# Kernel optimization log

Measured on AMD Instinct MI355X. Metric: run time of the kernel, lower is better.

The kernel has to match this reference:

```python
import jax, jax.numpy as jnp
import numpy as np

N = 50000      # nodes
E = 800000     # edges (before self-loops)
IN = 128       # input_dim
H = 4          # heads in conv1
C = 128        # per-head channels
G = 128        # num graphs in batch
OUT = 8        # output_dim
EPS = 1e-5


def layer_norm(x, g, b):
    mu = jnp.mean(x, axis=-1, keepdims=True)
    var = jnp.var(x, axis=-1, keepdims=True)
    return (x - mu) * jax.lax.rsqrt(var + EPS) * g + b


def gat_conv(x, src, dst, W, att_src, att_dst, bias, heads, ch):
    n = x.shape[0]
    h = (x @ W).reshape(n, heads, ch)                      # [N,H,C]
    a_src = jnp.einsum('nhc,hc->nh', h, att_src)           # [N,H]
    a_dst = jnp.einsum('nhc,hc->nh', h, att_dst)
    e = jax.nn.leaky_relu(a_src[src] + a_dst[dst], 0.2)    # [E,H]
    e_max = jax.ops.segment_max(e, dst, num_segments=n)
    e_max = jnp.where(jnp.isfinite(e_max), e_max, 0.0)
    ex = jnp.exp(e - e_max[dst])
    denom = jax.ops.segment_sum(ex, dst, num_segments=n)
    alpha = ex / (denom[dst] + 1e-16)                      # segment softmax over dst
    msg = h[src] * alpha[:, :, None]                       # [E,H,C]
    out = jax.ops.segment_sum(msg, dst, num_segments=n)    # [N,H,C]
    return out.reshape(n, heads * ch) + bias


def _forward(x, edge_index, batch, params):
    (W1, as1, ad1, b1, g1, be1, W2, as2, ad2, b2, g2, be2,
     rW1, rb1, rg, rbe, rW2, rb2) = params
    # add self-loops (PyG GATConv default)
    loop = jnp.arange(N)
    src = jnp.concatenate([edge_index[0], loop])
    dst = jnp.concatenate([edge_index[1], loop])
    h1 = jax.nn.relu(layer_norm(gat_conv(x, src, dst, W1, as1, ad1, b1, H, C), g1, be1))
    h2 = jax.nn.relu(layer_norm(gat_conv(h1, src, dst, W2, as2, ad2, b2, 1, C), g2, be2))
    # global mean pool
    sums = jax.ops.segment_sum(h2, batch, num_segments=G)
    cnt = jax.ops.segment_sum(jnp.ones((N, 1), h2.dtype), batch, num_segments=G)
    pooled = sums / jnp.maximum(cnt, 1.0)
    r = jax.nn.relu(layer_norm(pooled @ rW1 + rb1, rg, rbe))
    return r @ rW2 + rb2                                   # [G, OUT]


def setup_inputs() -> dict:
    key = jax.random.key(0)
    ks = jax.random.split(key, 24)
    s = 0.05
    return {
        'x': jax.random.normal(ks[0], (N, IN), jnp.float32),
        'edge_index': jax.random.randint(ks[1], (2, E), 0, N),
        'edge_weight': jax.random.uniform(ks[2], (E,), jnp.float32),
        'batch': jnp.sort(jax.random.randint(ks[3], (N,), 0, G)),
        'W1': jax.random.normal(ks[4], (IN, H * C), jnp.float32) * s,
        'att_src1': jax.random.normal(ks[5], (H, C), jnp.float32) * s,
        'att_dst1': jax.random.normal(ks[6], (H, C), jnp.float32) * s,
        'b1': jnp.zeros((H * C,), jnp.float32),
        'g1': jnp.ones((H * C,), jnp.float32),
        'be1': jnp.zeros((H * C,), jnp.float32),
        'W2': jax.random.normal(ks[7], (H * C, C), jnp.float32) * s,
        'att_src2': jax.random.normal(ks[8], (1, C), jnp.float32) * s,
        'att_dst2': jax.random.normal(ks[9], (1, C), jnp.float32) * s,
        'b2': jnp.zeros((C,), jnp.float32),
        'g2': jnp.ones((C,), jnp.float32),
        'be2': jnp.zeros((C,), jnp.float32),
        'rW1': jax.random.normal(ks[10], (C, 32), jnp.float32) * s,
        'rb1': jnp.zeros((32,), jnp.float32),
        'rg': jnp.ones((32,), jnp.float32),
        'rbe': jnp.zeros((32,), jnp.float32),
        'rW2': jax.random.normal(ks[11], (32, OUT), jnp.float32) * s,
        'rb2': jnp.zeros((OUT,), jnp.float32),
    }


def reference(x, edge_index, edge_weight, batch, W1, att_src1, att_dst1, b1, g1, be1,
              W2, att_src2, att_dst2, b2, g2, be2, rW1, rb1, rg, rbe, rW2, rb2):
    # edge_weight is accepted but unused, matching the original forward
    params = (W1, att_src1, att_dst1, b1, g1, be1, W2, att_src2, att_dst2, b2, g2, be2,
              rW1, rb1, rg, rbe, rW2, rb2)
    return _forward(x, edge_index, batch, params)
```

## Files before the change

kernel.cpp:

```cpp
#include <hip/hip_runtime.h>
#include <math.h>

#define HEADS 4
#define CH 128
#define HC 512
#define GRAPHS 128
#define OUT_DIM 8

typedef unsigned short u16;
typedef unsigned int u32;
typedef short short8 __attribute__((ext_vector_type(8)));
typedef float f32x4 __attribute__((ext_vector_type(4)));

__device__ inline u16 f2b(float f) {
  u32 u = __float_as_uint(f);
  u32 r = u + 0x7FFFu + ((u >> 16) & 1u);
  return (u16)(r >> 16);
}
__device__ inline float blo(u32 d) { return __uint_as_float(d << 16); }
__device__ inline float bhi(u32 d) { return __uint_as_float(d & 0xffff0000u); }
__device__ inline float lrelu(float v) { return v > 0.f ? v : 0.2f * v; }
__device__ inline int rdl(int v, int l) { return __builtin_amdgcn_readlane(v, l); }
__device__ inline float rdlf(float v, int l) {
  return __int_as_float(__builtin_amdgcn_readlane(__float_as_int(v), l));
}

__global__ void k_count(const int* __restrict__ ei, int* __restrict__ counts, int E, int N) {
  int i = blockIdx.x * blockDim.x + threadIdx.x;
  int total = E + N;
  if (i >= total) return;
  int dst = (i < E) ? ei[E + i] : (i - E);
  atomicAdd(&counts[dst], 1);
}

__global__ __launch_bounds__(256) void k_scanA(const int* __restrict__ counts,
                                               int* __restrict__ bsum, int N) {
  __shared__ int sh[256];
  int b = blockIdx.x, t = threadIdx.x, i = b * 256 + t;
  sh[t] = (i < N) ? counts[i] : 0;
  __syncthreads();
  for (int off = 128; off; off >>= 1) {
    if (t < off) sh[t] += sh[t + off];
    __syncthreads();
  }
  if (t == 0) bsum[b] = sh[0];
}

__global__ __launch_bounds__(1024) void k_scanB(const int* __restrict__ bsum,
                                                int* __restrict__ boff, int nb) {
  __shared__ int sh[1024];
  int t = threadIdx.x;
  sh[t] = (t < nb) ? bsum[t] : 0;
  __syncthreads();
  for (int off = 1; off < 1024; off <<= 1) {
    int v = sh[t];
    int u = (t >= off) ? sh[t - off] : 0;
    __syncthreads();
    sh[t] = v + u;
    __syncthreads();
  }
  if (t < nb) boff[t] = (t == 0) ? 0 : sh[t - 1];
}

__global__ __launch_bounds__(256) void k_scanC(const int* __restrict__ counts,
                                               const int* __restrict__ boff,
                                               int* __restrict__ indptr,
                                               int* __restrict__ cursor, int N) {
  __shared__ int sh[256];
  int b = blockIdx.x, t = threadIdx.x, i = b * 256 + t;
  int v = (i < N) ? counts[i] : 0;
  sh[t] = v;
  __syncthreads();
  for (int off = 1; off < 256; off <<= 1) {
    int a = sh[t];
    int u = (t >= off) ? sh[t - off] : 0;
    __syncthreads();
    sh[t] = a + u;
    __syncthreads();
  }
  if (i < N) {
    int excl = boff[b] + sh[t] - v;
    indptr[i] = excl;
    cursor[i] = excl;
    if (i == N - 1) indptr[N] = excl + v;
  }
}

__global__ void k_scatter(const int* __restrict__ ei, int* __restrict__ cursor,
                          int* __restrict__ srcs, int E, int N) {
  int i = blockIdx.x * blockDim.x + threadIdx.x;
  int total = E + N;
  if (i >= total) return;
  int src, dst;
  if (i < E) { src = ei[i]; dst = ei[E + i]; } else { src = i - E; dst = i - E; }
  int pos = atomicAdd(&cursor[dst], 1);
  srcs[pos] = src;
}

__global__ void k_wt(const float* __restrict__ W, u16* __restrict__ Wt, int K, int Nc) {
  int i = blockIdx.x * blockDim.x + threadIdx.x;
  if (i >= K * Nc) return;
  int n = i / K, k = i - n * K;
  Wt[i] = f2b(W[(size_t)k * Nc + n]);
}

__global__ __launch_bounds__(256) void k_ws(const float* __restrict__ W1,
                                            const float* __restrict__ as1,
                                            const float* __restrict__ ad1,
                                            float* __restrict__ ws) {
  int t = threadIdx.x;
  #pragma unroll
  for (int r = 0; r < 4; r++) {
    int idx = r * 256 + t;
    int k = idx >> 3, o = idx & 7, h = o & 3;
    const float* av = ((o < 4) ? as1 : ad1) + h * CH;
    const float* wrow = W1 + (size_t)k * HC + h * CH;
    float s = 0.f;
    for (int c = 0; c < CH; c++) s += wrow[c] * av[c];
    ws[idx] = s;
  }
}

__global__ void k_prep(const float* __restrict__ x, const float* __restrict__ ws,
                       u32* __restrict__ xb, float4* __restrict__ sa1,
                       float4* __restrict__ da1, int N) {
  int n = blockIdx.x * (blockDim.x >> 6) + (threadIdx.x >> 6);
  int lane = threadIdx.x & 63;
  if (n >= N) return;
  float2 v = ((const float2*)(x + (size_t)n * 128))[lane];
  xb[(size_t)n * 64 + lane] = (u32)f2b(v.x) | ((u32)f2b(v.y) << 16);
  const float* w0 = ws + (2 * lane) * 8;
  const float* w1 = ws + (2 * lane + 1) * 8;
  float p[8];
  #pragma unroll
  for (int o = 0; o < 8; o++) p[o] = v.x * w0[o] + v.y * w1[o];
  #pragma unroll
  for (int off = 32; off; off >>= 1)
    #pragma unroll
    for (int o = 0; o < 8; o++) p[o] += __shfl_xor(p[o], off);
  if (lane == 0) {
    sa1[n] = make_float4(p[0], p[1], p[2], p[3]);
    da1[n] = make_float4(p[4], p[5], p[6], p[7]);
  }
}

__global__ __launch_bounds__(256) void k_aggx(
    const u32* __restrict__ xb, const int* __restrict__ indptr,
    const int* __restrict__ srcs, const float4* __restrict__ as1,
    const float4* __restrict__ ad1, u32* __restrict__ aggx, int N) {
  int t = threadIdx.x;
  int lane = t & 63, wid = t >> 6;
  int n0 = blockIdx.x * 8 + wid * 2;
  if (n0 >= N) return;
  int n1 = n0 + 1;
  bool has1 = n1 < N;
  int beg0 = indptr[n0], end0 = indptr[n0 + 1];
  int beg1 = end0, end1 = has1 ? indptr[n1 + 1] : end0;
  int deg0 = end0 - beg0, deg1 = end1 - beg1;
  float4 ad0 = ad1[n0];
  float4 adv1 = has1 ? ad1[n1] : make_float4(0.f, 0.f, 0.f, 0.f);

  if (deg0 <= 64 && deg1 <= 64) {
    int s0 = 0, s1 = 0;
    float w0[4] = {}, w1[4] = {};
    if (lane < deg0) {
      s0 = srcs[beg0 + lane];
      float4 a = as1[s0];
      w0[0] = __expf(lrelu(a.x + ad0.x)); w0[1] = __expf(lrelu(a.y + ad0.y));
      w0[2] = __expf(lrelu(a.z + ad0.z)); w0[3] = __expf(lrelu(a.w + ad0.w));
    }
    if (lane < deg1) {
      s1 = srcs[beg1 + lane];
      float4 a = as1[s1];
      w1[0] = __expf(lrelu(a.x + adv1.x)); w1[1] = __expf(lrelu(a.y + adv1.y));
      w1[2] = __expf(lrelu(a.z + adv1.z)); w1[3] = __expf(lrelu(a.w + adv1.w));
    }
    float e0[4] = {}, e1[4] = {};
    float c0[4][2] = {}, c1[4][2] = {};
    int dmax = deg0 > deg1 ? deg0 : deg1;
    int dpad = (dmax + 3) & ~3;
    for (int j = 0; j < dpad; j += 4) {
      u32 d[4], e[4];
      #pragma unroll
      for (int u = 0; u < 4; u++) d[u] = xb[(size_t)rdl(s0, j + u) * 64 + lane];
      #pragma unroll
      for (int u = 0; u < 4; u++) e[u] = xb[(size_t)rdl(s1, j + u) * 64 + lane];
      #pragma unroll
      for (int h = 0; h < 4; h++) {
        #pragma unroll
        for (int u = 0; u < 4; u++) {
          float a = rdlf(w0[h], j + u);
          e0[h] += a; c0[h][0] += a * blo(d[u]); c0[h][1] += a * bhi(d[u]);
          float b = rdlf(w1[h], j + u);
          e1[h] += b; c1[h][0] += b * blo(e[u]); c1[h][1] += b * bhi(e[u]);
        }
      }
    }
    {
      u32* orow = aggx + (size_t)n0 * 256;
      #pragma unroll
      for (int h = 0; h < 4; h++) {
        float iv = 1.f / (e0[h] + 1e-16f);
        orow[h * 64 + lane] = (u32)f2b(c0[h][0] * iv) | ((u32)f2b(c0[h][1] * iv) << 16);
      }
    }
    if (has1) {
      u32* orow = aggx + (size_t)n1 * 256;
      #pragma unroll
      for (int h = 0; h < 4; h++) {
        float iv = 1.f / (e1[h] + 1e-16f);
        orow[h * 64 + lane] = (u32)f2b(c1[h][0] * iv) | ((u32)f2b(c1[h][1] * iv) << 16);
      }
    }
    return;
  }
  for (int pass = 0; pass < 2; pass++) {
    if (pass == 1 && !has1) break;
    int n = pass ? n1 : n0;
    int beg = pass ? beg1 : beg0;
    int end = pass ? end1 : end0;
    float4 ad = pass ? adv1 : ad0;
    float e0[4] = {};
    float c0[4][2] = {};
    for (int base = beg; base < end; base += 64) {
      int cnt = min(64, end - base);
      int sreg = 0;
      float w0[4] = {};
      if (lane < cnt) {
        sreg = srcs[base + lane];
        float4 a = as1[sreg];
        w0[0] = __expf(lrelu(a.x + ad.x)); w0[1] = __expf(lrelu(a.y + ad.y));
        w0[2] = __expf(lrelu(a.z + ad.z)); w0[3] = __expf(lrelu(a.w + ad.w));
      }
      int cpad = (cnt + 1) & ~1;
      for (int j = 0; j < cpad; j += 2) {
        u32 dA = xb[(size_t)rdl(sreg, j) * 64 + lane];
        u32 dB = xb[(size_t)rdl(sreg, j + 1) * 64 + lane];
        float xA0 = blo(dA), xA1 = bhi(dA), xB0 = blo(dB), xB1 = bhi(dB);
        #pragma unroll
        for (int h = 0; h < 4; h++) {
          float a = rdlf(w0[h], j), b = rdlf(w0[h], j + 1);
          e0[h] += a + b;
          c0[h][0] += a * xA0 + b * xB0;
          c0[h][1] += a * xA1 + b * xB1;
        }
      }
    }
    u32* orow = aggx + (size_t)n * 256;
    #pragma unroll
    for (int h = 0; h < 4; h++) {
      float iv = 1.f / (e0[h] + 1e-16f);
      orow[h * 64 + lane] = (u32)f2b(c0[h][0] * iv) | ((u32)f2b(c0[h][1] * iv) << 16);
    }
  }
}

__global__ __launch_bounds__(256) void k_gemm_head(
    const u16* __restrict__ A,
    const u16* __restrict__ Bt,
    const float* __restrict__ bias,
    u16* __restrict__ C,
    int M) {
  __shared__ u16 As[128 * 64];
  __shared__ u16 Bs[128 * 64];
  int t = threadIdx.x;
  int lane = t & 63, wid = t >> 6;
  int wr = wid >> 1, wc = wid & 1;
  int r0 = blockIdx.x * 128;
  int hh = blockIdx.y;
  const u16* Ah = A + hh * 128;
  const u16* Bh = Bt + (size_t)hh * 128 * 128;
  int lr = lane & 15, lk = lane >> 4;
  f32x4 acc[4][4] = {};
  for (int kt = 0; kt < 128; kt += 64) {
    #pragma unroll
    for (int it = 0; it < 4; it++) {
      int q = wid * 4096 + it * 1024 + lane * 16;
      int row = q >> 7;
      int soff = ((q >> 4) & 7) ^ (row & 7);
      {
        int gr = r0 + row; if (gr >= M) gr = M - 1;
        const u16* gp = Ah + (size_t)gr * 512 + kt + soff * 8;
        __builtin_amdgcn_global_load_lds(
            (const __attribute__((address_space(1))) void*)gp,
            (__attribute__((address_space(3))) void*)((char*)As + wid * 4096 + it * 1024),
            16, 0, 0);
      }
      {
        const u16* gp = Bh + (size_t)row * 128 + kt + soff * 8;
        __builtin_amdgcn_global_load_lds(
            (const __attribute__((address_space(1))) void*)gp,
            (__attribute__((address_space(3))) void*)((char*)Bs + wid * 4096 + it * 1024),
            16, 0, 0);
      }
    }
    __syncthreads();
    const char* Ab = (const char*)As;
    const char* Bb = (const char*)Bs;
    #pragma unroll
    for (int kk = 0; kk < 2; kk++) {
      short8 a[4], b[4];
      #pragma unroll
      for (int m = 0; m < 4; m++) {
        int row = wr * 64 + m * 16 + lr;
        int off = (row << 7) + kk * 64 + lk * 16;
        off ^= (row & 7) << 4;
        a[m] = *(const short8*)(Ab + off);
      }
      #pragma unroll
      for (int nn = 0; nn < 4; nn++) {
        int row = wc * 64 + nn * 16 + lr;
        int off = (row << 7) + kk * 64 + lk * 16;
        off ^= (row & 7) << 4;
        b[nn] = *(const short8*)(Bb + off);
      }
      #pragma unroll
      for (int m = 0; m < 4; m++)
        #pragma unroll
        for (int nn = 0; nn < 4; nn++)
          acc[m][nn] = __builtin_amdgcn_mfma_f32_16x16x32_bf16(a[m], b[nn], acc[m][nn], 0, 0, 0);
    }
    __syncthreads();
  }
  #pragma unroll
  for (int m = 0; m < 4; m++)
    #pragma unroll
    for (int nn = 0; nn < 4; nn++)
      #pragma unroll
      for (int r = 0; r < 4; r++) {
        int row = r0 + wr * 64 + m * 16 + lk * 4 + r;
        if (row < M) {
          int gcol = hh * 128 + wc * 64 + nn * 16 + lr;
          C[(size_t)row * 512 + gcol] = f2b(acc[m][nn][r] + bias[gcol]);
        }
      }
}

__global__ __launch_bounds__(256) void k_ln512(const u16* __restrict__ raw,
                                               const float* __restrict__ gam,
                                               const float* __restrict__ bet,
                                               u16* __restrict__ out, int N) {
  int n = blockIdx.x * 4 + (threadIdx.x >> 6);
  int lane = threadIdx.x & 63;
  if (n >= N) return;
  const uint4* r = (const uint4*)(raw + (size_t)n * 512);
  uint4 q = r[lane];
  float v[8];
  v[0] = blo(q.x); v[1] = bhi(q.x); v[2] = blo(q.y); v[3] = bhi(q.y);
  v[4] = blo(q.z); v[5] = bhi(q.z); v[6] = blo(q.w); v[7] = bhi(q.w);
  float s1 = 0.f, s2 = 0.f;
  #pragma unroll
  for (int j = 0; j < 8; j++) { s1 += v[j]; s2 += v[j] * v[j]; }
  #pragma unroll
  for (int off = 32; off; off >>= 1) {
    s1 += __shfl_xor(s1, off);
    s2 += __shfl_xor(s2, off);
  }
  float mean = s1 * (1.f / 512.f);
  float var = s2 * (1.f / 512.f) - mean * mean;
  float rs = rsqrtf(var + 1e-5f);
  u32 o[4];
  #pragma unroll
  for (int j = 0; j < 4; j++) {
    int ch = lane * 8 + 2 * j;
    float y0 = fmaxf((v[2 * j] - mean) * rs * gam[ch] + bet[ch], 0.f);
    float y1 = fmaxf((v[2 * j + 1] - mean) * rs * gam[ch + 1] + bet[ch + 1], 0.f);
    o[j] = (u32)f2b(y0) | ((u32)f2b(y1) << 16);
  }
  ((uint4*)(out + (size_t)n * 512))[lane] = make_uint4(o[0], o[1], o[2], o[3]);
}

__global__ __launch_bounds__(256) void k_gemm_bf16(
    const u16* __restrict__ A, const u16* __restrict__ Bt,
    u16* __restrict__ C, int M, int Nc, int K) {
  __shared__ u16 As[128 * 64];
  __shared__ u16 Bs[128 * 64];
  int t = threadIdx.x;
  int lane = t & 63, wid = t >> 6;
  int wr = wid >> 1, wc = wid & 1;
  int r0 = blockIdx.x * 128, c0 = blockIdx.y * 128;
  int lr = lane & 15, lk = lane >> 4;
  f32x4 acc[4][4] = {};
  for (int kt = 0; kt < K; kt += 64) {
    #pragma unroll
    for (int it = 0; it < 4; it++) {
      int q = wid * 4096 + it * 1024 + lane * 16;
      int row = q >> 7;
      int soff = ((q >> 4) & 7) ^ (row & 7);
      {
        int gr = r0 + row; if (gr >= M) gr = M - 1;
        const u16* gp = A + (size_t)gr * K + kt + soff * 8;
        __builtin_amdgcn_global_load_lds(
            (const __attribute__((address_space(1))) void*)gp,
            (__attribute__((address_space(3))) void*)((char*)As + wid * 4096 + it * 1024),
            16, 0, 0);
      }
      {
        int gn = c0 + row;
        const u16* gp = Bt + (size_t)gn * K + kt + soff * 8;
        __builtin_amdgcn_global_load_lds(
            (const __attribute__((address_space(1))) void*)gp,
            (__attribute__((address_space(3))) void*)((char*)Bs + wid * 4096 + it * 1024),
            16, 0, 0);
      }
    }
    __syncthreads();
    const char* Ab = (const char*)As;
    const char* Bb = (const char*)Bs;
    #pragma unroll
    for (int kk = 0; kk < 2; kk++) {
      short8 a[4], b[4];
      #pragma unroll
      for (int m = 0; m < 4; m++) {
        int row = wr * 64 + m * 16 + lr;
        int off = (row << 7) + kk * 64 + lk * 16;
        off ^= (row & 7) << 4;
        a[m] = *(const short8*)(Ab + off);
      }
      #pragma unroll
      for (int nn = 0; nn < 4; nn++) {
        int row = wc * 64 + nn * 16 + lr;
        int off = (row << 7) + kk * 64 + lk * 16;
        off ^= (row & 7) << 4;
        b[nn] = *(const short8*)(Bb + off);
      }
      #pragma unroll
      for (int m = 0; m < 4; m++)
        #pragma unroll
        for (int nn = 0; nn < 4; nn++)
          acc[m][nn] = __builtin_amdgcn_mfma_f32_16x16x32_bf16(a[m], b[nn], acc[m][nn], 0, 0, 0);
    }
    __syncthreads();
  }
  #pragma unroll
  for (int m = 0; m < 4; m++)
    #pragma unroll
    for (int nn = 0; nn < 4; nn++)
      #pragma unroll
      for (int r = 0; r < 4; r++) {
        int row = r0 + wr * 64 + m * 16 + lk * 4 + r;
        if (row < M) {
          int col = c0 + wc * 64 + nn * 16 + lr;
          C[(size_t)row * Nc + col] = f2b(acc[m][nn][r]);
        }
      }
}

__global__ void k_att_h1(const u16* __restrict__ hm, const float* __restrict__ att_s,
                         const float* __restrict__ att_d, float* __restrict__ s_out,
                         float* __restrict__ d_out, int N) {
  int n = blockIdx.x * (blockDim.x >> 6) + (threadIdx.x >> 6);
  int lane = threadIdx.x & 63;
  if (n >= N) return;
  const u32* row = (const u32*)(hm + (size_t)n * CH);
  u32 d = row[lane];
  float x0 = blo(d), x1 = bhi(d);
  float ps = x0 * att_s[2 * lane] + x1 * att_s[2 * lane + 1];
  float pd = x0 * att_d[2 * lane] + x1 * att_d[2 * lane + 1];
  #pragma unroll
  for (int off = 32; off; off >>= 1) {
    ps += __shfl_xor(ps, off);
    pd += __shfl_xor(pd, off);
  }
  if (lane == 0) { s_out[n] = ps; d_out[n] = pd; }
}

__global__ __launch_bounds__(256) void k_agg2f(
    const u32* __restrict__ raw2, const int* __restrict__ indptr,
    const int* __restrict__ srcs, const float* __restrict__ as2,
    const float* __restrict__ ad2, const float* __restrict__ bias,
    const float* __restrict__ gam, const float* __restrict__ bet,
    float* __restrict__ h2, int N) {
  int t = threadIdx.x;
  int lane = t & 63, wid = t >> 6;
  int n0 = blockIdx.x * 8 + wid * 2;
  if (n0 >= N) return;
  int n1 = n0 + 1;
  bool has1 = n1 < N;
  int beg0 = indptr[n0], end0 = indptr[n0 + 1];
  int beg1 = end0, end1 = has1 ? indptr[n1 + 1] : end0;
  int deg0 = end0 - beg0, deg1 = end1 - beg1;
  float adv0 = ad2[n0];
  float adv1 = has1 ? ad2[n1] : 0.f;
  float ds0 = 0.f, ds1 = 0.f;
  float a00 = 0.f, a01 = 0.f, a10 = 0.f, a11 = 0.f;

  if (deg0 <= 64 && deg1 <= 64) {
    int s0 = 0, s1r = 0;
    float w0 = 0.f, w1 = 0.f;
    if (lane < deg0) { s0 = srcs[beg0 + lane]; w0 = __expf(lrelu(as2[s0] + adv0)); }
    if (lane < deg1) { s1r = srcs[beg1 + lane]; w1 = __expf(lrelu(as2[s1r] + adv1)); }
    int dmax = deg0 > deg1 ? deg0 : deg1;
    int dpad = (dmax + 7) & ~7;
    for (int j = 0; j < dpad; j += 8) {
      u32 d[8], e[8];
      #pragma unroll
      for (int u = 0; u < 8; u++) d[u] = raw2[(size_t)rdl(s0, j + u) * 64 + lane];
      #pragma unroll
      for (int u = 0; u < 8; u++) e[u] = raw2[(size_t)rdl(s1r, j + u) * 64 + lane];
      #pragma unroll
      for (int u = 0; u < 8; u++) {
        float a = rdlf(w0, j + u);
        ds0 += a; a00 += a * blo(d[u]); a01 += a * bhi(d[u]);
        float b = rdlf(w1, j + u);
        ds1 += b; a10 += b * blo(e[u]); a11 += b * bhi(e[u]);
      }
    }
  } else {
    for (int pass = 0; pass < 2; pass++) {
      if (pass == 1 && !has1) break;
      int beg = pass ? beg1 : beg0;
      int end = pass ? end1 : end0;
      float adv = pass ? adv1 : adv0;
      for (int base = beg; base < end; base += 64) {
        int cnt = min(64, end - base);
        int sreg = 0;
        float w = 0.f;
        if (lane < cnt) { sreg = srcs[base + lane]; w = __expf(lrelu(as2[sreg] + adv)); }
        int cpad = (cnt + 3) & ~3;
        for (int j = 0; j < cpad; j += 4) {
          u32 dA = raw2[(size_t)rdl(sreg, j) * 64 + lane];
          u32 dB = raw2[(size_t)rdl(sreg, j + 1) * 64 + lane];
          u32 dC = raw2[(size_t)rdl(sreg, j + 2) * 64 + lane];
          u32 dD = raw2[(size_t)rdl(sreg, j + 3) * 64 + lane];
          float wA = rdlf(w, j), wB = rdlf(w, j + 1);
          float wC = rdlf(w, j + 2), wD = rdlf(w, j + 3);
          float lo = wA * blo(dA) + wB * blo(dB) + wC * blo(dC) + wD * blo(dD);
          float hi = wA * bhi(dA) + wB * bhi(dB) + wC * bhi(dC) + wD * bhi(dD);
          float sw = (wA + wB) + (wC + wD);
          if (pass) { ds1 += sw; a10 += lo; a11 += hi; }
          else      { ds0 += sw; a00 += lo; a01 += hi; }
        }
      }
    }
  }

  float inv0 = 1.f / (ds0 + 1e-16f);
  float v00 = a00 * inv0 + bias[2 * lane];
  float v01 = a01 * inv0 + bias[2 * lane + 1];
  float s1a = v00 + v01, s2a = v00 * v00 + v01 * v01;
  float inv1 = 1.f / (ds1 + 1e-16f);
  float v10 = a10 * inv1 + bias[2 * lane];
  float v11 = a11 * inv1 + bias[2 * lane + 1];
  float s1b = v10 + v11, s2b = v10 * v10 + v11 * v11;
  #pragma unroll
  for (int off = 32; off; off >>= 1) {
    s1a += __shfl_xor(s1a, off);
    s2a += __shfl_xor(s2a, off);
    s1b += __shfl_xor(s1b, off);
    s2b += __shfl_xor(s2b, off);
  }
  {
    float mean = s1a * (1.f / 128.f);
    float var = s2a * (1.f / 128.f) - mean * mean;
    float rs = rsqrtf(var + 1e-5f);
    float y0 = fmaxf((v00 - mean) * rs * gam[2 * lane] + bet[2 * lane], 0.f);
    float y1 = fmaxf((v01 - mean) * rs * gam[2 * lane + 1] + bet[2 * lane + 1], 0.f);
    ((float2*)(h2 + (size_t)n0 * 128))[lane] = make_float2(y0, y1);
  }
  if (has1) {
    float mean = s1b * (1.f / 128.f);
    float var = s2b * (1.f / 128.f) - mean * mean;
    float rs = rsqrtf(var + 1e-5f);
    float y0 = fmaxf((v10 - mean) * rs * gam[2 * lane] + bet[2 * lane], 0.f);
    float y1 = fmaxf((v11 - mean) * rs * gam[2 * lane + 1] + bet[2 * lane + 1], 0.f);
    ((float2*)(h2 + (size_t)n1 * 128))[lane] = make_float2(y0, y1);
  }
}

__global__ __launch_bounds__(256) void k_head(const float* __restrict__ h2,
    const int* __restrict__ batch, int N,
    const float* __restrict__ rW1, const float* __restrict__ rb1,
    const float* __restrict__ rg, const float* __restrict__ rbe,
    const float* __restrict__ rW2, const float* __restrict__ rb2,
    float* __restrict__ outp) {
  int g = blockIdx.x, t = threadIdx.x;
  int ch = t & 127, half = t >> 7;
  __shared__ float part[2][128];
  __shared__ float pl[128];
  __shared__ float yv[32];
  __shared__ float rv[32];
  __shared__ float mv[2];
  __shared__ int sseg[2];
  if (t == 0) {
    int lo = 0, hi = N;
    while (lo < hi) { int mid = (lo + hi) >> 1; if (batch[mid] < g) lo = mid + 1; else hi = mid; }
    int lo2 = lo, hi2 = N;
    while (lo2 < hi2) { int mid = (lo2 + hi2) >> 1; if (batch[mid] < g + 1) lo2 = mid + 1; else hi2 = mid; }
    sseg[0] = lo; sseg[1] = lo2;
  }
  __syncthreads();
  int lo = sseg[0], hi = sseg[1];
  float s = 0.f;
  int n = lo + half;
  for (; n + 8 <= hi; n += 8) {
    s += h2[(size_t)n * 128 + ch] + h2[(size_t)(n + 2) * 128 + ch]
       + h2[(size_t)(n + 4) * 128 + ch] + h2[(size_t)(n + 6) * 128 + ch];
  }
  for (; n < hi; n += 2) s += h2[(size_t)n * 128 + ch];
  part[half][ch] = s;
  __syncthreads();
  float cnt = fmaxf((float)(hi - lo), 1.f);
  if (t < 128) pl[t] = (part[0][t] + part[1][t]) / cnt;
  __syncthreads();
  if (t < 32) {
    float sum = rb1[t];
    for (int c = 0; c < 128; c++) sum += pl[c] * rW1[c * 32 + t];
    yv[t] = sum;
  }
  __syncthreads();
  if (t == 0) {
    float sm = 0.f, sq = 0.f;
    for (int j = 0; j < 32; j++) { sm += yv[j]; sq += yv[j] * yv[j]; }
    float mean = sm / 32.f;
    float var = sq / 32.f - mean * mean;
    mv[0] = mean; mv[1] = rsqrtf(var + 1e-5f);
  }
  __syncthreads();
  if (t < 32) {
    float y = (yv[t] - mv[0]) * mv[1] * rg[t] + rbe[t];
    rv[t] = fmaxf(y, 0.f);
  }
  __syncthreads();
  if (t < OUT_DIM) {
    float sum = rb2[t];
    for (int j = 0; j < 32; j++) sum += rv[j] * rW2[j * 8 + t];
    outp[g * 8 + t] = sum;
  }
}

extern "C" void kernel_launch(void* const* d_in, const int* in_sizes, int n_in,
                              void* d_out, int out_size, void* d_ws, size_t ws_size,
                              hipStream_t stream) {
  const float* x    = (const float*)d_in[0];
  const int*   ei   = (const int*)d_in[1];
  const int*   batch= (const int*)d_in[3];
  const float* W1   = (const float*)d_in[4];
  const float* as1w = (const float*)d_in[5];
  const float* ad1w = (const float*)d_in[6];
  const float* b1   = (const float*)d_in[7];
  const float* g1   = (const float*)d_in[8];
  const float* be1  = (const float*)d_in[9];
  const float* W2   = (const float*)d_in[10];
  const float* as2w = (const float*)d_in[11];
  const float* ad2w = (const float*)d_in[12];
  const float* b2   = (const float*)d_in[13];
  const float* g2   = (const float*)d_in[14];
  const float* be2  = (const float*)d_in[15];
  const float* rW1  = (const float*)d_in[16];
  const float* rb1  = (const float*)d_in[17];
  const float* rg   = (const float*)d_in[18];
  const float* rbe  = (const float*)d_in[19];
  const float* rW2  = (const float*)d_in[20];
  const float* rb2  = (const float*)d_in[21];

  int N = in_sizes[0] / 128;
  int E = in_sizes[1] / 2;
  int ET = E + N;
  int nb = (N + 255) / 256;

  char* p = (char*)d_ws;
  u16* x_b   = (u16*)p; p += (size_t)N * 128 * 2;
  u16* aggx  = (u16*)p; p += (size_t)N * 512 * 2;
  u16* raw1  = (u16*)p; p += (size_t)N * 512 * 2;
  u16* h1_b  = (u16*)p; p += (size_t)N * 512 * 2;
  u16* raw2b = (u16*)p; p += (size_t)N * 128 * 2;
  float* h2  = (float*)p; p += (size_t)N * 128 * 4;
  u16* W1t   = (u16*)p; p += 512 * 128 * 2;
  u16* W2t   = (u16*)p; p += 128 * 512 * 2;
  float* ws  = (float*)p; p += 128 * 8 * 4;
  float* sa1 = (float*)p; p += (size_t)N * 4 * 4;
  float* da1 = (float*)p; p += (size_t)N * 4 * 4;
  float* sa2 = (float*)p; p += (size_t)N * 4;
  float* da2 = (float*)p; p += (size_t)N * 4;
  int* counts = (int*)p; p += (size_t)N * 4;
  int* indptr = (int*)p; p += (size_t)(N + 1) * 4;
  int* cursor = (int*)p; p += (size_t)N * 4;
  int* bsum   = (int*)p; p += (size_t)nb * 4;
  int* boff   = (int*)p; p += (size_t)nb * 4;
  int* srcs   = (int*)p; p += (size_t)ET * 4;

  hipMemsetAsync(counts, 0, (size_t)N * sizeof(int), stream);

  int eb = (ET + 255) / 256;
  k_count<<<eb, 256, 0, stream>>>(ei, counts, E, N);
  k_scanA<<<nb, 256, 0, stream>>>(counts, bsum, N);
  k_scanB<<<1, 1024, 0, stream>>>(bsum, boff, nb);
  k_scanC<<<nb, 256, 0, stream>>>(counts, boff, indptr, cursor, N);
  k_scatter<<<eb, 256, 0, stream>>>(ei, cursor, srcs, E, N);

  k_wt<<<(512 * 128 + 255) / 256, 256, 0, stream>>>(W1, W1t, 128, 512);
  k_wt<<<(512 * 128 + 255) / 256, 256, 0, stream>>>(W2, W2t, 512, 128);
  k_ws<<<1, 256, 0, stream>>>(W1, as1w, ad1w, ws);
  k_prep<<<(N + 3) / 4, 256, 0, stream>>>(x, ws, (u32*)x_b, (float4*)sa1, (float4*)da1, N);

  k_aggx<<<(N + 7) / 8, 256, 0, stream>>>((const u32*)x_b, indptr, srcs,
                                          (const float4*)sa1, (const float4*)da1,
                                          (u32*)aggx, N);
  dim3 gridh((N + 127) / 128, 4);
  k_gemm_head<<<gridh, 256, 0, stream>>>(aggx, W1t, b1, raw1, N);
  k_ln512<<<(N + 3) / 4, 256, 0, stream>>>(raw1, g1, be1, h1_b, N);

  dim3 grid2((N + 127) / 128, 1);
  k_gemm_bf16<<<grid2, 256, 0, stream>>>(h1_b, W2t, raw2b, N, 128, 512);
  k_att_h1<<<(N + 3) / 4, 256, 0, stream>>>(raw2b, as2w, ad2w, sa2, da2, N);
  k_agg2f<<<(N + 7) / 8, 256, 0, stream>>>((const u32*)raw2b, indptr, srcs, sa2, da2,
                                           b2, g2, be2, h2, N);

  k_head<<<GRAPHS, 256, 0, stream>>>(h2, batch, N, rW1, rb1, rg, rbe, rW2, rb2,
                                     (float*)d_out);
}
```

Before: 358.2 us.

## Fuse prep kernels and split dual-node aggregation loops by degree

```diff
diff --git a/kernel.cpp b/kernel.cpp
--- a/kernel.cpp
+++ b/kernel.cpp
@@ -11,6 +11,7 @@
 typedef unsigned int u32;
 typedef short short8 __attribute__((ext_vector_type(8)));
 typedef float f32x4 __attribute__((ext_vector_type(4)));
+typedef float f32x2 __attribute__((ext_vector_type(2)));
 
 __device__ inline u16 f2b(float f) {
   u32 u = __float_as_uint(f);
@@ -19,18 +20,13 @@
 }
 __device__ inline float blo(u32 d) { return __uint_as_float(d << 16); }
 __device__ inline float bhi(u32 d) { return __uint_as_float(d & 0xffff0000u); }
+__device__ inline f32x2 bunpack(u32 d) {
+  f32x2 r; r.x = blo(d); r.y = bhi(d); return r;
+}
 __device__ inline float lrelu(float v) { return v > 0.f ? v : 0.2f * v; }
 __device__ inline int rdl(int v, int l) { return __builtin_amdgcn_readlane(v, l); }
 __device__ inline float rdlf(float v, int l) {
   return __int_as_float(__builtin_amdgcn_readlane(__float_as_int(v), l));
-}
-
-__global__ void k_count(const int* __restrict__ ei, int* __restrict__ counts, int E, int N) {
-  int i = blockIdx.x * blockDim.x + threadIdx.x;
-  int total = E + N;
-  if (i >= total) return;
-  int dst = (i < E) ? ei[E + i] : (i - E);
-  atomicAdd(&counts[dst], 1);
 }
 
 __global__ __launch_bounds__(256) void k_scanA(const int* __restrict__ counts,
@@ -97,21 +93,24 @@
   srcs[pos] = src;
 }
 
-__global__ void k_wt(const float* __restrict__ W, u16* __restrict__ Wt, int K, int Nc) {
-  int i = blockIdx.x * blockDim.x + threadIdx.x;
-  if (i >= K * Nc) return;
-  int n = i / K, k = i - n * K;
-  Wt[i] = f2b(W[(size_t)k * Nc + n]);
-}
-
-__global__ __launch_bounds__(256) void k_ws(const float* __restrict__ W1,
-                                            const float* __restrict__ as1,
-                                            const float* __restrict__ ad1,
-                                            float* __restrict__ ws) {
-  int t = threadIdx.x;
-  #pragma unroll
-  for (int r = 0; r < 4; r++) {
-    int idx = r * 256 + t;
+__global__ __launch_bounds__(256) void k_wprep(const float* __restrict__ W1,
+                                               const float* __restrict__ W2,
+                                               const float* __restrict__ as1,
+                                               const float* __restrict__ ad1,
+                                               u16* __restrict__ W1t,
+                                               u16* __restrict__ W2t,
+                                               float* __restrict__ ws) {
+  int b = blockIdx.x, t = threadIdx.x;
+  if (b < 256) {
+    int i = b * 256 + t;
+    int n = i >> 7, k = i & 127;
+    W1t[i] = f2b(W1[(size_t)k * HC + n]);
+  } else if (b < 512) {
+    int i = (b - 256) * 256 + t;
+    int n = i >> 9, k = i & 511;
+    W2t[i] = f2b(W2[(size_t)k * CH + n]);
+  } else {
+    int idx = (b - 512) * 256 + t;
     int k = idx >> 3, o = idx & 7, h = o & 3;
     const float* av = ((o < 4) ? as1 : ad1) + h * CH;
     const float* wrow = W1 + (size_t)k * HC + h * CH;
@@ -121,10 +120,20 @@
   }
 }
 
-__global__ void k_prep(const float* __restrict__ x, const float* __restrict__ ws,
-                       u32* __restrict__ xb, float4* __restrict__ sa1,
-                       float4* __restrict__ da1, int N) {
-  int n = blockIdx.x * (blockDim.x >> 6) + (threadIdx.x >> 6);
+__global__ void k_count_prep(const int* __restrict__ ei, int* __restrict__ counts,
+                             int E, int N, int eb,
+                             const float* __restrict__ x, const float* __restrict__ ws,
+                             u32* __restrict__ xb, float4* __restrict__ sa1,
+                             float4* __restrict__ da1) {
+  if ((int)blockIdx.x < eb) {
+    int i = blockIdx.x * 256 + threadIdx.x;
+    int total = E + N;
+    if (i >= total) return;
+    int dst = (i < E) ? ei[E + i] : (i - E);
+    atomicAdd(&counts[dst], 1);
+    return;
+  }
+  int n = (blockIdx.x - eb) * 4 + (threadIdx.x >> 6);
   int lane = threadIdx.x & 63;
   if (n >= N) return;
   float2 v = ((const float2*)(x + (size_t)n * 128))[lane];
@@ -175,33 +184,67 @@
       w1[0] = __expf(lrelu(a.x + adv1.x)); w1[1] = __expf(lrelu(a.y + adv1.y));
       w1[2] = __expf(lrelu(a.z + adv1.z)); w1[3] = __expf(lrelu(a.w + adv1.w));
     }
-    float e0[4] = {}, e1[4] = {};
-    float c0[4][2] = {}, c1[4][2] = {};
-    int dmax = deg0 > deg1 ? deg0 : deg1;
-    int dpad = (dmax + 3) & ~3;
-    for (int j = 0; j < dpad; j += 4) {
+    f32x2 c0[4] = {}, c1[4] = {};
+    int dboth = (deg0 < deg1 ? deg0 : deg1) & ~3;
+    int j = 0;
+    for (; j < dboth; j += 4) {
       u32 d[4], e[4];
       #pragma unroll
       for (int u = 0; u < 4; u++) d[u] = xb[(size_t)rdl(s0, j + u) * 64 + lane];
       #pragma unroll
       for (int u = 0; u < 4; u++) e[u] = xb[(size_t)rdl(s1, j + u) * 64 + lane];
       #pragma unroll
-      for (int h = 0; h < 4; h++) {
+      for (int u = 0; u < 4; u++) {
+        f32x2 xv = bunpack(d[u]);
+        f32x2 yv = bunpack(e[u]);
         #pragma unroll
-        for (int u = 0; u < 4; u++) {
-          float a = rdlf(w0[h], j + u);
-          e0[h] += a; c0[h][0] += a * blo(d[u]); c0[h][1] += a * bhi(d[u]);
-          float b = rdlf(w1[h], j + u);
-          e1[h] += b; c1[h][0] += b * blo(e[u]); c1[h][1] += b * bhi(e[u]);
+        for (int h = 0; h < 4; h++) {
+          c0[h] += xv * rdlf(w0[h], j + u);
+          c1[h] += yv * rdlf(w1[h], j + u);
         }
       }
+    }
+    int pad0 = (deg0 + 3) & ~3;
+    for (int ja = j; ja < pad0; ja += 4) {
+      u32 d[4];
+      #pragma unroll
+      for (int u = 0; u < 4; u++) d[u] = xb[(size_t)rdl(s0, ja + u) * 64 + lane];
+      #pragma unroll
+      for (int u = 0; u < 4; u++) {
+        f32x2 xv = bunpack(d[u]);
+        #pragma unroll
+        for (int h = 0; h < 4; h++) c0[h] += xv * rdlf(w0[h], ja + u);
+      }
+    }
+    int pad1 = (deg1 + 3) & ~3;
+    for (int jb = j; jb < pad1; jb += 4) {
+      u32 e[4];
+      #pragma unroll
+      for (int u = 0; u < 4; u++) e[u] = xb[(size_t)rdl(s1, jb + u) * 64 + lane];
+      #pragma unroll
+      for (int u = 0; u < 4; u++) {
+        f32x2 yv = bunpack(e[u]);
+        #pragma unroll
+        for (int h = 0; h < 4; h++) c1[h] += yv * rdlf(w1[h], jb + u);
+      }
+    }
+    float e0[4], e1[4];
+    #pragma unroll
+    for (int h = 0; h < 4; h++) {
+      float v0 = w0[h], v1 = w1[h];
+      #pragma unroll
+      for (int off = 32; off; off >>= 1) {
+        v0 += __shfl_xor(v0, off);
+        v1 += __shfl_xor(v1, off);
+      }
+      e0[h] = v0; e1[h] = v1;
     }
     {
       u32* orow = aggx + (size_t)n0 * 256;
       #pragma unroll
       for (int h = 0; h < 4; h++) {
         float iv = 1.f / (e0[h] + 1e-16f);
-        orow[h * 64 + lane] = (u32)f2b(c0[h][0] * iv) | ((u32)f2b(c0[h][1] * iv) << 16);
+        orow[h * 64 + lane] = (u32)f2b(c0[h].x * iv) | ((u32)f2b(c0[h].y * iv) << 16);
       }
     }
     if (has1) {
@@ -209,7 +252,7 @@
       #pragma unroll
       for (int h = 0; h < 4; h++) {
         float iv = 1.f / (e1[h] + 1e-16f);
-        orow[h * 64 + lane] = (u32)f2b(c1[h][0] * iv) | ((u32)f2b(c1[h][1] * iv) << 16);
+        orow[h * 64 + lane] = (u32)f2b(c1[h].x * iv) | ((u32)f2b(c1[h].y * iv) << 16);
       }
     }
     return;
@@ -221,7 +264,7 @@
     int end = pass ? end1 : end0;
     float4 ad = pass ? adv1 : ad0;
     float e0[4] = {};
-    float c0[4][2] = {};
+    f32x2 c0[4] = {};
     for (int base = beg; base < end; base += 64) {
       int cnt = min(64, end - base);
       int sreg = 0;
@@ -236,13 +279,13 @@
       for (int j = 0; j < cpad; j += 2) {
         u32 dA = xb[(size_t)rdl(sreg, j) * 64 + lane];
         u32 dB = xb[(size_t)rdl(sreg, j + 1) * 64 + lane];
-        float xA0 = blo(dA), xA1 = bhi(dA), xB0 = blo(dB), xB1 = bhi(dB);
+        f32x2 xA = bunpack(dA), xB = bunpack(dB);
         #pragma unroll
         for (int h = 0; h < 4; h++) {
           float a = rdlf(w0[h], j), b = rdlf(w0[h], j + 1);
           e0[h] += a + b;
-          c0[h][0] += a * xA0 + b * xB0;
-          c0[h][1] += a * xA1 + b * xB1;
+          c0[h] += xA * a;
+          c0[h] += xB * b;
         }
       }
     }
@@ -250,7 +293,7 @@
     #pragma unroll
     for (int h = 0; h < 4; h++) {
       float iv = 1.f / (e0[h] + 1e-16f);
-      orow[h * 64 + lane] = (u32)f2b(c0[h][0] * iv) | ((u32)f2b(c0[h][1] * iv) << 16);
+      orow[h * 64 + lane] = (u32)f2b(c0[h].x * iv) | ((u32)f2b(c0[h].y * iv) << 16);
     }
   }
 }
@@ -483,16 +526,16 @@
   float adv0 = ad2[n0];
   float adv1 = has1 ? ad2[n1] : 0.f;
   float ds0 = 0.f, ds1 = 0.f;
-  float a00 = 0.f, a01 = 0.f, a10 = 0.f, a11 = 0.f;
+  f32x2 acc0 = {0.f, 0.f}, acc1 = {0.f, 0.f};
 
   if (deg0 <= 64 && deg1 <= 64) {
     int s0 = 0, s1r = 0;
     float w0 = 0.f, w1 = 0.f;
     if (lane < deg0) { s0 = srcs[beg0 + lane]; w0 = __expf(lrelu(as2[s0] + adv0)); }
     if (lane < deg1) { s1r = srcs[beg1 + lane]; w1 = __expf(lrelu(as2[s1r] + adv1)); }
-    int dmax = deg0 > deg1 ? deg0 : deg1;
-    int dpad = (dmax + 7) & ~7;
-    for (int j = 0; j < dpad; j += 8) {
+    int dboth = (deg0 < deg1 ? deg0 : deg1) & ~7;
+    int j = 0;
+    for (; j < dboth; j += 8) {
       u32 d[8], e[8];
       #pragma unroll
       for (int u = 0; u < 8; u++) d[u] = raw2[(size_t)rdl(s0, j + u) * 64 + lane];
@@ -500,12 +543,33 @@
       for (int u = 0; u < 8; u++) e[u] = raw2[(size_t)rdl(s1r, j + u) * 64 + lane];
       #pragma unroll
       for (int u = 0; u < 8; u++) {
-        float a = rdlf(w0, j + u);
-        ds0 += a; a00 += a * blo(d[u]); a01 += a * bhi(d[u]);
-        float b = rdlf(w1, j + u);
-        ds1 += b; a10 += b * blo(e[u]); a11 += b * bhi(e[u]);
-      }
-    }
+        acc0 += bunpack(d[u]) * rdlf(w0, j + u);
+        acc1 += bunpack(e[u]) * rdlf(w1, j + u);
+      }
+    }
+    int pad0 = (deg0 + 3) & ~3;
+    for (int ja = j; ja < pad0; ja += 4) {
+      u32 d[4];
+      #pragma unroll
+      for (int u = 0; u < 4; u++) d[u] = raw2[(size_t)rdl(s0, ja + u) * 64 + lane];
+      #pragma unroll
+      for (int u = 0; u < 4; u++) acc0 += bunpack(d[u]) * rdlf(w0, ja + u);
+    }
+    int pad1 = (deg1 + 3) & ~3;
+    for (int jb = j; jb < pad1; jb += 4) {
+      u32 e[4];
+      #pragma unroll
+      for (int u = 0; u < 4; u++) e[u] = raw2[(size_t)rdl(s1r, jb + u) * 64 + lane];
+      #pragma unroll
+      for (int u = 0; u < 4; u++) acc1 += bunpack(e[u]) * rdlf(w1, jb + u);
+    }
+    float v0 = w0, v1 = w1;
+    #pragma unroll
+    for (int off = 32; off; off >>= 1) {
+      v0 += __shfl_xor(v0, off);
+      v1 += __shfl_xor(v1, off);
+    }
+    ds0 = v0; ds1 = v1;
   } else {
     for (int pass = 0; pass < 2; pass++) {
       if (pass == 1 && !has1) break;
@@ -525,23 +589,25 @@
           u32 dD = raw2[(size_t)rdl(sreg, j + 3) * 64 + lane];
           float wA = rdlf(w, j), wB = rdlf(w, j + 1);
           float wC = rdlf(w, j + 2), wD = rdlf(w, j + 3);
-          float lo = wA * blo(dA) + wB * blo(dB) + wC * blo(dC) + wD * blo(dD);
-          float hi = wA * bhi(dA) + wB * bhi(dB) + wC * bhi(dC) + wD * bhi(dD);
+          f32x2 s = bunpack(dA) * wA;
+          s += bunpack(dB) * wB;
+          s += bunpack(dC) * wC;
+          s += bunpack(dD) * wD;
           float sw = (wA + wB) + (wC + wD);
-          if (pass) { ds1 += sw; a10 += lo; a11 += hi; }
-          else      { ds0 += sw; a00 += lo; a01 += hi; }
+          if (pass) { ds1 += sw; acc1 += s; }
+          else      { ds0 += sw; acc0 += s; }
         }
       }
     }
   }
 
   float inv0 = 1.f / (ds0 + 1e-16f);
-  float v00 = a00 * inv0 + bias[2 * lane];
-  float v01 = a01 * inv0 + bias[2 * lane + 1];
+  float v00 = acc0.x * inv0 + bias[2 * lane];
+  float v01 = acc0.y * inv0 + bias[2 * lane + 1];
   float s1a = v00 + v01, s2a = v00 * v00 + v01 * v01;
   float inv1 = 1.f / (ds1 + 1e-16f);
-  float v10 = a10 * inv1 + bias[2 * lane];
-  float v11 = a11 * inv1 + bias[2 * lane + 1];
+  float v10 = acc1.x * inv1 + bias[2 * lane];
+  float v11 = acc1.y * inv1 + bias[2 * lane + 1];
   float s1b = v10 + v11, s2b = v10 * v10 + v11 * v11;
   #pragma unroll
   for (int off = 32; off; off >>= 1) {
@@ -683,16 +749,17 @@
   hipMemsetAsync(counts, 0, (size_t)N * sizeof(int), stream);
 
   int eb = (ET + 255) / 256;
-  k_count<<<eb, 256, 0, stream>>>(ei, counts, E, N);
+
+  k_wprep<<<516, 256, 0, stream>>>(W1, W2, as1w, ad1w, W1t, W2t, ws);
+
+  int pb = (N + 3) / 4;
+  k_count_prep<<<eb + pb, 256, 0, stream>>>(ei, counts, E, N, eb, x, ws,
+                                            (u32*)x_b, (float4*)sa1, (float4*)da1);
+
   k_scanA<<<nb, 256, 0, stream>>>(counts, bsum, N);
   k_scanB<<<1, 1024, 0, stream>>>(bsum, boff, nb);
   k_scanC<<<nb, 256, 0, stream>>>(counts, boff, indptr, cursor, N);
   k_scatter<<<eb, 256, 0, stream>>>(ei, cursor, srcs, E, N);
-
-  k_wt<<<(512 * 128 + 255) / 256, 256, 0, stream>>>(W1, W1t, 128, 512);
-  k_wt<<<(512 * 128 + 255) / 256, 256, 0, stream>>>(W2, W2t, 512, 128);
-  k_ws<<<1, 256, 0, stream>>>(W1, as1w, ad1w, ws);
-  k_prep<<<(N + 3) / 4, 256, 0, stream>>>(x, ws, (u32*)x_b, (float4*)sa1, (float4*)da1, N);
 
   k_aggx<<<(N + 7) / 8, 256, 0, stream>>>((const u32*)x_b, indptr, srcs,
                                           (const float4*)sa1, (const float4*)da1,
```

Result: faster. 324.7 us (-9.4%).
